# Performance work log

Hardware: AMD Instinct MI355X
Metric: run time of the kernel (lower is better)

The kernel has to match this reference:

```python
import jax, jax.numpy as jnp
import numpy as np

POOLSCALE = 4  # HSA: avg-pool kernel/stride = (scale, scale*4)

def _avg_pool(x, kh, kw):
    # kernel == stride and dims divisible -> exact reshape-mean pooling
    B, C, H, W = x.shape
    return x.reshape(B, C, H // kh, kh, W // kw, kw).mean(axis=(3, 5))

def setup_inputs() -> dict:
    key = jax.random.key(0)
    k1, k2, k3 = jax.random.split(key, 3)
    shape = (4, 64, 192, 192)
    return {
        "K": jax.random.normal(k1, shape, dtype=jnp.float32),
        "Q": jax.random.normal(k2, shape, dtype=jnp.float32),
        "V": jax.random.normal(k3, shape, dtype=jnp.float32),
    }

def reference(K, Q, V):
    B, C, H, W = Q.shape
    kh, kw = POOLSCALE, POOLSCALE * 4
    Qp = Q.reshape(B, C, H * W).transpose(0, 2, 1)          # [B, HW, C]
    Kp = _avg_pool(K, kh, kw)                               # [B, C, h, w]
    Kp = Kp.reshape(B, C, -1)                               # [B, C, hw_p]
    Vp = _avg_pool(V, kh, kw).reshape(B, C, -1)             # [B, C, hw_p]
    scores = jnp.einsum('bnc,bcm->bnm', Qp, Kp)             # [B, HW, hw_p]
    attn = jax.nn.softmax(scores, axis=1)                   # softmax over query dim (dim=1), as in torch code
    out = jnp.einsum('bcm,bnm->bcn', Vp, attn)              # V_pie @ attn^T -> [B, C, HW]
    return out.reshape(B, C, H, W)
```

## Files before the change

kernel.cpp:

```cpp
#include <hip/hip_runtime.h>
#include <stdint.h>

#define BB 4
#define CC 64
#define HH 192
#define WW 192
#define HWN (HH*WW)
#define KH 4
#define KW 16
#define PW (WW/KW)
#define MP ((HH/KH)*(WW/KW))
#define MITER (MP/64)
#define NBTOT (HWN/32)
#define NUNIT (HWN/64)
#define NGRP 36
#define NT256 (HWN/256)
#define SCALE_W 65536.0f
#define INV_SCALE (1.0f/65536.0f)
#define LOG2E 1.44269504088896f

typedef _Float16 half8 __attribute__((ext_vector_type(8)));
typedef _Float16 half4 __attribute__((ext_vector_type(4)));
typedef float floatx4 __attribute__((ext_vector_type(4)));

static __device__ __forceinline__ void gload16(const void* g, void* l) {
  __builtin_amdgcn_global_load_lds((const __attribute__((address_space(1))) void*)g,
                                   (__attribute__((address_space(3))) void*)l, 16, 0, 0);
}
#define WAITCNT_VM(N) asm volatile("s_waitcnt vmcnt(" #N ")" ::: "memory")

static __device__ __forceinline__ float fexp2(float x) {
#if __has_builtin(__builtin_amdgcn_exp2f)
  return __builtin_amdgcn_exp2f(x);
#else
  return __expf(x * 0.6931471805599453f);
#endif
}


__global__ __launch_bounds__(256) void prep2_kernel(
    const float* __restrict__ Kin, const float* __restrict__ Vin,
    const float* __restrict__ Q,
    _Float16* __restrict__ kptF, float* __restrict__ vp,
    _Float16* __restrict__ qF) {
  __shared__ float lsf[9216];
  int tid = threadIdx.x;
  if (blockIdx.x < BB * CC) {
    int bc = blockIdx.x;
    int b = bc / CC, c = bc % CC;
    int ks = c >> 5, lhi = (c >> 3) & 3, e = c & 7;
    {
      const float4* kp4 = (const float4*)(Kin + (size_t)bc * HWN);
#pragma unroll
      for (int it = 0; it < 36; ++it) {
        int idx = it * 256 + tid;
        float4 v = kp4[idx];
        lsf[idx] = v.x + v.y + v.z + v.w;
      }
      __syncthreads();
      for (int ci = tid; ci < MP; ci += 256) {
        int ph = ci / 12, pw = ci % 12;
        float s = 0.f;
#pragma unroll
        for (int r = 0; r < 4; ++r)
#pragma unroll
          for (int q = 0; q < 4; ++q)
            s += lsf[(ph * 4 + r) * 48 + pw * 4 + q];
        s *= (1.0f / 64.0f);
        int mi = ci >> 6, w = ci & 63, mf = w >> 4, l15 = w & 15;
        int lane = lhi * 16 + l15;
        kptF[((((b * MITER + mi) * 4 + mf) * 2 + ks) * 64 + lane) * 8 + e] =
            (_Float16)(s * LOG2E);
      }
      __syncthreads();
    }
    {
      const float4* vp4 = (const float4*)(Vin + (size_t)bc * HWN);
#pragma unroll
      for (int it = 0; it < 36; ++it) {
        int idx = it * 256 + tid;
        float4 v = vp4[idx];
        lsf[idx] = v.x + v.y + v.z + v.w;
      }
      __syncthreads();
      for (int ci = tid; ci < MP; ci += 256) {
        int ph = ci / 12, pw = ci % 12;
        float s = 0.f;
#pragma unroll
        for (int r = 0; r < 4; ++r)
#pragma unroll
          for (int q = 0; q < 4; ++q)
            s += lsf[(ph * 4 + r) * 48 + pw * 4 + q];
        vp[(size_t)bc * MP + ci] = s * (1.0f / 64.0f);
      }
    }
  } else {
    int qb = blockIdx.x - BB * CC;
    int b = qb / NT256, nt = qb % NT256;
    int n0 = nt * 256;
    unsigned short* lsu = (unsigned short*)lsf;
#pragma unroll
    for (int it = 0; it < 16; ++it) {
      int idx = it * 256 + tid;
      int c = idx >> 6, nn = idx & 63;
      float4 v = *((const float4*)(Q + (size_t)(b * CC + c) * HWN + n0) + nn);
      half4 hh = {(_Float16)v.x, (_Float16)v.y, (_Float16)v.z, (_Float16)v.w};
      *(half4*)(&lsu[c * 260 + nn * 4]) = hh;
    }
    __syncthreads();
    int lane = tid & 63, wv = tid >> 6;
    int l15 = lane & 15, lhi = lane >> 4;
#pragma unroll
    for (int nbl2 = 0; nbl2 < 2; ++nbl2) {
      int nbl = wv * 2 + nbl2;
      int nb = nt * 8 + nbl;
#pragma unroll
      for (int ks = 0; ks < 2; ++ks)
#pragma unroll
        for (int nf = 0; nf < 2; ++nf) {
          int nl = nbl * 32 + nf * 16 + l15;
          int c0 = ks * 32 + lhi * 8;
          half8 h;
#pragma unroll
          for (int e = 0; e < 8; ++e)
            h[e] = *(const _Float16*)&lsu[(c0 + e) * 260 + nl];
          *(half8*)(qF + (size_t)((b * NBTOT + nb) * 4 + ks * 2 + nf) * 512 +
                    lane * 8) = h;
        }
    }
  }
}

__global__ __launch_bounds__(256) void colsum_qf2_kernel(
    const _Float16* __restrict__ qF, const _Float16* __restrict__ kptF,
    float* __restrict__ part) {
  int tid = threadIdx.x;
  int lane = tid & 63;
  int l15 = lane & 15;
  int u = blockIdx.x * 4 + (tid >> 6);
  int b = u / NUNIT;
  int un = u % NUNIT;

  const _Float16* qc = qF + (size_t)((b * NBTOT + un * 2) * 4) * 512 + lane * 8;
  half8 af[2][2][2];
#pragma unroll
  for (int nb = 0; nb < 2; ++nb)
#pragma unroll
    for (int ks = 0; ks < 2; ++ks)
#pragma unroll
      for (int nf = 0; nf < 2; ++nf)
        af[nb][nf][ks] = *(const half8*)(qc + (nb * 4 + ks * 2 + nf) * 512);

  const _Float16* kb = kptF + b * MITER * 8 * 512;
  floatx4 zero = {0.f, 0.f, 0.f, 0.f};
  float* pout = part + (size_t)(b * NUNIT + un) * MP;

#pragma unroll
  for (int mi = 0; mi < MITER; ++mi) {
    half8 bfr[4][2];
#pragma unroll
    for (int mf = 0; mf < 4; ++mf)
#pragma unroll
      for (int ks = 0; ks < 2; ++ks)
        bfr[mf][ks] = *(const half8*)(kb + ((mi * 4 + mf) * 2 + ks) * 512 + lane * 8);

    float s0 = 0.f, s1 = 0.f, s2 = 0.f, s3 = 0.f;
#pragma unroll
    for (int nb = 0; nb < 2; ++nb) {
      floatx4 sacc[2][4];
#pragma unroll
      for (int nf = 0; nf < 2; ++nf)
#pragma unroll
        for (int mf = 0; mf < 4; ++mf) sacc[nf][mf] = zero;
      __builtin_amdgcn_s_setprio(1);
#pragma unroll
      for (int ks = 0; ks < 2; ++ks)
#pragma unroll
        for (int nf = 0; nf < 2; ++nf)
#pragma unroll
          for (int mf = 0; mf < 4; ++mf)
            sacc[nf][mf] = __builtin_amdgcn_mfma_f32_16x16x32_f16(
                af[nb][nf][ks], bfr[mf][ks], sacc[nf][mf], 0, 0, 0);
      __builtin_amdgcn_s_setprio(0);
#pragma unroll
      for (int nf = 0; nf < 2; ++nf)
#pragma unroll
        for (int r = 0; r < 4; ++r) {
          s0 += fexp2(sacc[nf][0][r]);
          s1 += fexp2(sacc[nf][1][r]);
          s2 += fexp2(sacc[nf][2][r]);
          s3 += fexp2(sacc[nf][3][r]);
        }
    }
    s0 += __shfl_xor(s0, 16); s0 += __shfl_xor(s0, 32);
    s1 += __shfl_xor(s1, 16); s1 += __shfl_xor(s1, 32);
    s2 += __shfl_xor(s2, 16); s2 += __shfl_xor(s2, 32);
    s3 += __shfl_xor(s3, 16); s3 += __shfl_xor(s3, 32);
    if (lane < 16) {
      float* p = pout + mi * 64;
      p[0 * 16 + l15] = s0;
      p[1 * 16 + l15] = s1;
      p[2 * 16 + l15] = s2;
      p[3 * 16 + l15] = s3;
    }
  }
}

__global__ __launch_bounds__(576) void colsum_reduceA_kernel(
    const float* __restrict__ part, float* __restrict__ part2) {
  int m = threadIdx.x;
  int g = blockIdx.x;
  int b = blockIdx.y;
  const float* p = part + (size_t)(b * NUNIT + g * 16) * MP + m;
  float a0 = 0.f, a1 = 0.f, a2 = 0.f, a3 = 0.f;
#pragma unroll
  for (int j = 0; j < 16; j += 4) {
    a0 += p[(size_t)(j + 0) * MP];
    a1 += p[(size_t)(j + 1) * MP];
    a2 += p[(size_t)(j + 2) * MP];
    a3 += p[(size_t)(j + 3) * MP];
  }
  part2[(size_t)(b * NGRP + g) * MP + m] = (a0 + a1) + (a2 + a3);
}

__global__ __launch_bounds__(256) void colsum_reduceB_kernel(
    const float* __restrict__ part2, float* __restrict__ colsum) {
  int t = blockIdx.x * 256 + threadIdx.x;
  int m = t % MP;
  int b = t / MP;
  const float* p = part2 + (size_t)b * NGRP * MP + m;
  float a0 = 0.f, a1 = 0.f, a2 = 0.f, a3 = 0.f;
#pragma unroll
  for (int g = 0; g < NGRP; g += 4) {
    a0 += p[(size_t)(g + 0) * MP];
    a1 += p[(size_t)(g + 1) * MP];
    a2 += p[(size_t)(g + 2) * MP];
    a3 += p[(size_t)(g + 3) * MP];
  }
  colsum[t] = (a0 + a1) + (a2 + a3);
}

__global__ __launch_bounds__(256) void wprep_kernel(
    const float* __restrict__ vp, const float* __restrict__ colsum,
    _Float16* __restrict__ wqF) {
  int t = blockIdx.x * 256 + threadIdx.x;
  int m = t % MP;
  int c = (t / MP) % CC;
  int b = t / (CC * MP);
  float w = vp[t] / colsum[b * MP + m] * SCALE_W;
  int cf = c >> 4, l15 = c & 15;
  int mi = m >> 6, wl = m & 63;
  int ks = wl >> 5, v = wl & 31;
  int lhi = (v & 15) >> 2;
  int e = (v >> 4) * 4 + (v & 3);
  int lane = lhi * 16 + l15;
  wqF[((((b * MITER + mi) * 4 + cf) * 2 + ks) * 64 + lane) * 8 + e] = (_Float16)w;
}

__global__ __launch_bounds__(256) void attn_v5_kernel(
    const _Float16* __restrict__ qF, const _Float16* __restrict__ kptF,
    const _Float16* __restrict__ wqF, float* __restrict__ out) {
  __shared__ char stg[3 * 16384];
  int b = blockIdx.y;
  int tid = threadIdx.x;
  int wv = tid >> 6;
  int lane = tid & 63;
  int l15 = lane & 15, lhi = lane >> 4;

  const _Float16* kb = kptF + b * MITER * 8 * 512;
  const _Float16* wb = wqF + b * MITER * 8 * 512;

#define STAGE_V5(tt, ss)                                                       \
  {                                                                            \
    int q0_ = wv * 4;                                                          \
    _Pragma("unroll") for (int j_ = 0; j_ < 4; ++j_) {                         \
      int q_ = q0_ + j_;                                                       \
      const _Float16* sp_ = (q_ < 8 ? kb + (tt) * 4096 + q_ * 512              \
                                    : wb + (tt) * 4096 + (q_ - 8) * 512) +     \
                            lane * 8;                                          \
      gload16(sp_, stg + (ss) * 16384 + q_ * 1024);                            \
    }                                                                          \
  }

  int nb0 = blockIdx.x * 8 + wv * 2;
  const _Float16* qc = qF + (size_t)((b * NBTOT + nb0) * 4) * 512 + lane * 8;
  half8 afrag[2][2][2];
#pragma unroll
  for (int j = 0; j < 2; ++j)
#pragma unroll
    for (int ks = 0; ks < 2; ++ks)
#pragma unroll
      for (int nf = 0; nf < 2; ++nf)
        afrag[j][nf][ks] = *(const half8*)(qc + (j * 4 + ks * 2 + nf) * 512);
  STAGE_V5(0, 0);
  STAGE_V5(1, 1);

  floatx4 zero = {0.f, 0.f, 0.f, 0.f};
  floatx4 oacc[2][4][2];
#pragma unroll
  for (int j = 0; j < 2; ++j)
#pragma unroll
    for (int cf = 0; cf < 4; ++cf)
#pragma unroll
      for (int nf = 0; nf < 2; ++nf) oacc[j][cf][nf] = zero;

#pragma unroll
  for (int mi = 0; mi < MITER; ++mi) {
    const int sc = mi % 3;
    if (mi < MITER - 1) { WAITCNT_VM(4); } else { WAITCNT_VM(0); }
    __builtin_amdgcn_sched_barrier(0);
    __builtin_amdgcn_s_barrier();
    if (mi + 2 < MITER) STAGE_V5(mi + 2, (mi + 2) % 3);

    half8 bfr[4][2];
#pragma unroll
    for (int mf = 0; mf < 4; ++mf)
#pragma unroll
      for (int ks = 0; ks < 2; ++ks)
        bfr[mf][ks] = *(const half8*)(stg + sc * 16384 + (mf * 2 + ks) * 1024 + lane * 16);
    half8 wfr[4][2];
#pragma unroll
    for (int cf = 0; cf < 4; ++cf)
#pragma unroll
      for (int ks = 0; ks < 2; ++ks)
        wfr[cf][ks] = *(const half8*)(stg + sc * 16384 + 8192 + (cf * 2 + ks) * 1024 + lane * 16);

#pragma unroll
    for (int j = 0; j < 2; ++j) {
      floatx4 sacc[4][2];
#pragma unroll
      for (int mf = 0; mf < 4; ++mf)
#pragma unroll
        for (int nf = 0; nf < 2; ++nf) sacc[mf][nf] = zero;
      __builtin_amdgcn_s_setprio(1);
#pragma unroll
      for (int ks = 0; ks < 2; ++ks)
#pragma unroll
        for (int mf = 0; mf < 4; ++mf)
#pragma unroll
          for (int nf = 0; nf < 2; ++nf)
            sacc[mf][nf] = __builtin_amdgcn_mfma_f32_16x16x32_f16(
                bfr[mf][ks], afrag[j][nf][ks], sacc[mf][nf], 0, 0, 0);
      __builtin_amdgcn_s_setprio(0);

#pragma unroll
      for (int ks = 0; ks < 2; ++ks) {
        half8 ef[2];
#pragma unroll
        for (int nf = 0; nf < 2; ++nf)
#pragma unroll
          for (int e = 0; e < 8; ++e)
            ef[nf][e] = (_Float16)fexp2(sacc[2 * ks + (e >> 2)][nf][e & 3]);
        __builtin_amdgcn_s_setprio(1);
#pragma unroll
        for (int cf = 0; cf < 4; ++cf)
#pragma unroll
          for (int nf = 0; nf < 2; ++nf)
            oacc[j][cf][nf] = __builtin_amdgcn_mfma_f32_16x16x32_f16(
                wfr[cf][ks], ef[nf], oacc[j][cf][nf], 0, 0, 0);
        __builtin_amdgcn_s_setprio(0);
      }
    }
  }

  float* ob = out + b * CC * HWN;
#pragma unroll
  for (int j = 0; j < 2; ++j)
#pragma unroll
    for (int cf = 0; cf < 4; ++cf)
#pragma unroll
      for (int nf = 0; nf < 2; ++nf)
#pragma unroll
        for (int r = 0; r < 4; ++r) {
          int c = cf * 16 + lhi * 4 + r;
          int n = (nb0 + j) * 32 + nf * 16 + l15;
          ob[c * HWN + n] = oacc[j][cf][nf][r] * INV_SCALE;
        }
}

extern "C" void kernel_launch(void* const* d_in, const int* in_sizes, int n_in,
                              void* d_out, int out_size, void* d_ws, size_t ws_size,
                              hipStream_t stream) {
  const float* K = (const float*)d_in[0];
  const float* Q = (const float*)d_in[1];
  const float* V = (const float*)d_in[2];
  float* out = (float*)d_out;
  char* ws = (char*)d_ws;
  _Float16* kptF  = (_Float16*)(ws);
  float*    vp    = (float*)(ws + 294912);
  _Float16* wqF   = (_Float16*)(ws + 294912 + 589824);
  float*    colsum = (float*)(ws + 294912 + 589824 + 294912);
  const size_t QF_OFF = 1204224;
  _Float16* qF = (_Float16*)(ws + QF_OFF);
  float* part  = out;
  float* part2 = out + 2097152;

  prep2_kernel<<<BB * CC + BB * NT256, 256, 0, stream>>>(K, V, Q, kptF, vp, qF);
  colsum_qf2_kernel<<<(BB * NUNIT) / 4, 256, 0, stream>>>(qF, kptF, part);
  colsum_reduceA_kernel<<<dim3(NGRP, BB), 576, 0, stream>>>(part, part2);
  colsum_reduceB_kernel<<<(BB * MP) / 256, 256, 0, stream>>>(part2, colsum);
  wprep_kernel<<<(BB * CC * MP) / 256, 256, 0, stream>>>(vp, colsum, wqF);
  attn_v5_kernel<<<dim3(NBTOT / 8, BB), 256, 0, stream>>>(qF, kptF, wqF, out);
}
```

Measured before the change: 82.45 us.

## Stream K/V/Q tiles into LDS via direct global-to-LDS loads in prep kernel

The prep kernel now loads K, V and Q data with global_load_lds (direct global-to-LDS DMA) instead of loading through registers and then storing to shared memory. K and V are processed in six row chunks, each with a horizontal-sum pass and then a pooling pass, and Q is staged as fp32 in two channel halves before the fp16 transposed fragments are written out. Shared memory use drops from 36 KB to 32 KB. The trade-off is extra barriers per chunk, and with tid<96 only 96 of 256 threads do the pooling step.

Result: no change. 83.55 us (+1.3%).

```diff
diff --git a/kernel.cpp b/kernel.cpp
--- a/kernel.cpp
+++ b/kernel.cpp
@@ -20,7 +20,6 @@
 #define LOG2E 1.44269504088896f
 
 typedef _Float16 half8 __attribute__((ext_vector_type(8)));
-typedef _Float16 half4 __attribute__((ext_vector_type(4)));
 typedef float floatx4 __attribute__((ext_vector_type(4)));
 
 static __device__ __forceinline__ void gload16(const void* g, void* l) {
@@ -38,95 +37,89 @@
 }
 
 
-__global__ __launch_bounds__(256) void prep2_kernel(
+__global__ __launch_bounds__(256) void prep3_kernel(
     const float* __restrict__ Kin, const float* __restrict__ Vin,
     const float* __restrict__ Q,
     _Float16* __restrict__ kptF, float* __restrict__ vp,
     _Float16* __restrict__ qF) {
-  __shared__ float lsf[9216];
+  __shared__ float lsf[8192];
   int tid = threadIdx.x;
+  int lane = tid & 63, wv = tid >> 6;
   if (blockIdx.x < BB * CC) {
     int bc = blockIdx.x;
     int b = bc / CC, c = bc % CC;
     int ks = c >> 5, lhi = (c >> 3) & 3, e = c & 7;
-    {
-      const float4* kp4 = (const float4*)(Kin + (size_t)bc * HWN);
-#pragma unroll
-      for (int it = 0; it < 36; ++it) {
-        int idx = it * 256 + tid;
-        float4 v = kp4[idx];
-        lsf[idx] = v.x + v.y + v.z + v.w;
-      }
-      __syncthreads();
-      for (int ci = tid; ci < MP; ci += 256) {
-        int ph = ci / 12, pw = ci % 12;
-        float s = 0.f;
-#pragma unroll
-        for (int r = 0; r < 4; ++r)
-#pragma unroll
-          for (int q = 0; q < 4; ++q)
-            s += lsf[(ph * 4 + r) * 48 + pw * 4 + q];
-        s *= (1.0f / 64.0f);
-        int mi = ci >> 6, w = ci & 63, mf = w >> 4, l15 = w & 15;
-        int lane = lhi * 16 + l15;
-        kptF[((((b * MITER + mi) * 4 + mf) * 2 + ks) * 64 + lane) * 8 + e] =
-            (_Float16)(s * LOG2E);
-      }
-      __syncthreads();
-    }
-    {
-      const float4* vp4 = (const float4*)(Vin + (size_t)bc * HWN);
-#pragma unroll
-      for (int it = 0; it < 36; ++it) {
-        int idx = it * 256 + tid;
-        float4 v = vp4[idx];
-        lsf[idx] = v.x + v.y + v.z + v.w;
-      }
-      __syncthreads();
-      for (int ci = tid; ci < MP; ci += 256) {
-        int ph = ci / 12, pw = ci % 12;
-        float s = 0.f;
-#pragma unroll
-        for (int r = 0; r < 4; ++r)
-#pragma unroll
-          for (int q = 0; q < 4; ++q)
-            s += lsf[(ph * 4 + r) * 48 + pw * 4 + q];
-        vp[(size_t)bc * MP + ci] = s * (1.0f / 64.0f);
+    const float* planes[2] = {Kin + (size_t)bc * HWN, Vin + (size_t)bc * HWN};
+#pragma unroll
+    for (int pl = 0; pl < 2; ++pl) {
+      const char* pb = (const char*)planes[pl];
+      for (int ch = 0; ch < 6; ++ch) {
+#pragma unroll
+        for (int j = 0; j < 6; ++j) {
+          int q = wv * 6 + j;
+          gload16(pb + ch * 24576 + q * 1024 + lane * 16, (char*)lsf + q * 1024);
+        }
+        __syncthreads();
+        float* hs = lsf + 6144;
+#pragma unroll
+        for (int it = 0; it < 6; ++it) {
+          int idx = it * 256 + tid;
+          floatx4 v = ((const floatx4*)lsf)[idx];
+          hs[idx] = (v[0] + v[1]) + (v[2] + v[3]);
+        }
+        __syncthreads();
+        if (tid < 96) {
+          int pr = tid / 12, pw = tid % 12;
+          float s = 0.f;
+#pragma unroll
+          for (int r = 0; r < 4; ++r)
+#pragma unroll
+            for (int q = 0; q < 4; ++q)
+              s += hs[(pr * 4 + r) * 48 + pw * 4 + q];
+          s *= (1.0f / 64.0f);
+          int m = (ch * 8 + pr) * PW + pw;
+          if (pl == 0) {
+            int mi = m >> 6, w = m & 63, mf = w >> 4, l15 = w & 15;
+            int ln = lhi * 16 + l15;
+            kptF[((((b * MITER + mi) * 4 + mf) * 2 + ks) * 64 + ln) * 8 + e] =
+                (_Float16)(s * LOG2E);
+          } else {
+            vp[(size_t)bc * MP + m] = s;
+          }
+        }
+        __syncthreads();
       }
     }
   } else {
     int qb = blockIdx.x - BB * CC;
     int b = qb / NT256, nt = qb % NT256;
     int n0 = nt * 256;
-    unsigned short* lsu = (unsigned short*)lsf;
-#pragma unroll
-    for (int it = 0; it < 16; ++it) {
-      int idx = it * 256 + tid;
-      int c = idx >> 6, nn = idx & 63;
-      float4 v = *((const float4*)(Q + (size_t)(b * CC + c) * HWN + n0) + nn);
-      half4 hh = {(_Float16)v.x, (_Float16)v.y, (_Float16)v.z, (_Float16)v.w};
-      *(half4*)(&lsu[c * 260 + nn * 4]) = hh;
-    }
-    __syncthreads();
-    int lane = tid & 63, wv = tid >> 6;
     int l15 = lane & 15, lhi = lane >> 4;
 #pragma unroll
-    for (int nbl2 = 0; nbl2 < 2; ++nbl2) {
-      int nbl = wv * 2 + nbl2;
-      int nb = nt * 8 + nbl;
-#pragma unroll
-      for (int ks = 0; ks < 2; ++ks)
+    for (int ks = 0; ks < 2; ++ks) {
+#pragma unroll
+      for (int j = 0; j < 8; ++j) {
+        int q = wv * 8 + j;
+        const float* src = Q + (size_t)(b * CC + ks * 32 + q) * HWN + n0;
+        gload16(src + lane * 4, (char*)lsf + q * 1024);
+      }
+      __syncthreads();
+#pragma unroll
+      for (int nbl2 = 0; nbl2 < 2; ++nbl2) {
+        int nbl = wv * 2 + nbl2;
+        int nb = nt * 8 + nbl;
 #pragma unroll
         for (int nf = 0; nf < 2; ++nf) {
           int nl = nbl * 32 + nf * 16 + l15;
-          int c0 = ks * 32 + lhi * 8;
           half8 h;
 #pragma unroll
           for (int e = 0; e < 8; ++e)
-            h[e] = *(const _Float16*)&lsu[(c0 + e) * 260 + nl];
+            h[e] = (_Float16)lsf[(lhi * 8 + e) * 256 + nl];
           *(half8*)(qF + (size_t)((b * NBTOT + nb) * 4 + ks * 2 + nf) * 512 +
                     lane * 8) = h;
         }
+      }
+      __syncthreads();
     }
   }
 }
@@ -395,7 +388,7 @@
   float* part  = out;
   float* part2 = out + 2097152;
 
-  prep2_kernel<<<BB * CC + BB * NT256, 256, 0, stream>>>(K, V, Q, kptF, vp, qF);
+  prep3_kernel<<<BB * CC + BB * NT256, 256, 0, stream>>>(K, V, Q, kptF, vp, qF);
   colsum_qf2_kernel<<<(BB * NUNIT) / 4, 256, 0, stream>>>(qF, kptF, part);
   colsum_reduceA_kernel<<<dim3(NGRP, BB), 576, 0, stream>>>(part, part2);
   colsum_reduceB_kernel<<<(BB * MP) / 256, 256, 0, stream>>>(part2, colsum);
```
